# Kernel optimization log

Hardware: AMD Instinct MI355X
Metric: run time of the kernel (lower is better)

The kernel has to match this reference:

```python
import jax, jax.numpy as jnp
import numpy as np

B, NUM, NVAR = 2048, 100, 11
NUM_OBS, NC = 10, 3
T_FIN = 10.0
RHO_OBS = 1.0; RHO_INEQ = 1.0; RHO_LANE = 1.0; RHO_PROJ = 1.0
W_SMOOTH = 20.0; W_VDES = 2.0; W_YDES = 1.0
A_EGO = 3.0; B_EGO = 1.5; MARGIN = 0.2
V_MIN = 0.001; V_MAX = 18.0; A_MAX = 6.0
MAXITER = 5
H = 256

def _basis():
    s = np.linspace(0.0, 1.0, NUM)
    j = np.arange(NVAR)
    P = s[:, None] ** j[None, :]
    Pd = np.zeros((NUM, NVAR)); Pdd = np.zeros((NUM, NVAR))
    Pd[:, 1:] = j[1:][None, :] * s[:, None] ** (j[1:] - 1)[None, :]
    Pdd[:, 2:] = (j[2:] * (j[2:] - 1))[None, :] * s[:, None] ** (j[2:] - 2)[None, :]
    return (jnp.asarray(P, jnp.float32), jnp.asarray(Pd / T_FIN, jnp.float32),
            jnp.asarray(Pdd / (T_FIN ** 2), jnp.float32))

P, PDOT, PDDOT = _basis()
A_EQ_X = jnp.stack([P[0], PDOT[0], PDDOT[0], P[-1]])   # [4, NVAR]
A_EQ_Y = jnp.stack([P[0], PDOT[0], PDDOT[0]])          # [3, NVAR]
PTP = P.T @ P

def _kkt_inv(Q, A):
    m = A.shape[0]
    K = jnp.concatenate([jnp.concatenate([Q, A.T], axis=1),
                         jnp.concatenate([A, jnp.zeros((m, m), jnp.float32)], axis=1)], axis=0)
    return jnp.linalg.inv(K)

# ADMM cost: rho_proj*I + smoothness + rho_obs*A_obs^T A_obs + rho_ineq*(Pdot^T Pdot + Pddot^T Pddot)
Q_COMMON = (RHO_PROJ + W_SMOOTH) * jnp.eye(NVAR, dtype=jnp.float32) \
    + RHO_OBS * NUM_OBS * NC * PTP \
    + RHO_INEQ * (PDOT.T @ PDOT + PDDOT.T @ PDDOT)
KKT_X = _kkt_inv(Q_COMMON, A_EQ_X)
KKT_Y = _kkt_inv(Q_COMMON + 2.0 * RHO_LANE * PTP, A_EQ_Y)   # A_lane = [P; -P]
# x_init QP (smoothness + v_des / y_des tracking)
Q_IX = W_SMOOTH * jnp.eye(NVAR, dtype=jnp.float32) + W_VDES * (PDOT.T @ PDOT)
KKT_IX = _kkt_inv(Q_IX, A_EQ_X)
KKT_IY = _kkt_inv(Q_IX + W_YDES * PTP, A_EQ_Y)


def _forward(init_state_ego, goal_des, closest_obs, psi_obs, dim_x_obs, dim_y_obs,
             y_ub, y_lb, gru_W_ih, gru_W_hh, gru_b, gru_h0,
             mlp_W1, mlp_b1, mlp_W2, mlp_b2):
    b = init_state_ego.shape[0]
    x0, y0, vx0, vy0, ax0, ay0 = (init_state_ego[:, i] for i in range(6))
    b_eq_x = jnp.stack([x0, vx0, ax0, goal_des[:, 0]], axis=1)   # [B,4]
    b_eq_y = jnp.stack([y0, vy0, ay0], axis=1)                    # [B,3]

    # ---- obstacle circle trajectories (static obstacles, vx=vy=0) ----
    xo = closest_obs[:, :NUM_OBS]; yo = closest_obs[:, NUM_OBS:2 * NUM_OBS]   # [B,O]
    r = jnp.stack([jnp.zeros_like(dim_x_obs),
                   (dim_x_obs - dim_y_obs) / 2,
                   -(dim_x_obs - dim_y_obs) / 2], axis=2)                      # [B,O,3]
    x_circ = xo[:, :, None] + r * jnp.cos(psi_obs)[:, :, None]                # [B,O,3]
    y_circ = yo[:, :, None] + r * jnp.sin(psi_obs)[:, :, None]
    shape4 = (b, NUM_OBS, NC, NUM)
    x_obs_f = jnp.broadcast_to(x_circ[..., None], shape4).reshape(b, -1)      # [B,O*C*T]
    y_obs_f = jnp.broadcast_to(y_circ[..., None], shape4).reshape(b, -1)
    rad = dim_y_obs / 2
    a_obs = jnp.broadcast_to((A_EGO + rad + MARGIN)[:, :, None, None], shape4).reshape(b, -1)
    b_obs = jnp.broadcast_to((B_EGO + rad + MARGIN)[:, :, None, None], shape4).reshape(b, -1)

    # ---- GRU context over obstacles -> learned lambda init ----
    feats = jnp.stack([xo, yo, dim_x_obs, dim_y_obs, psi_obs], axis=2)        # [B,O,5]
    def gru_step(h, x):
        gx = x @ gru_W_ih + gru_b
        gh = h @ gru_W_hh
        z = jax.nn.sigmoid(gx[:, :H] + gh[:, :H])
        rg = jax.nn.sigmoid(gx[:, H:2 * H] + gh[:, H:2 * H])
        n = jnp.tanh(gx[:, 2 * H:] + rg * gh[:, 2 * H:])
        return (1.0 - z) * n + z * h, None
    hT, _ = jax.lax.scan(gru_step, jnp.broadcast_to(gru_h0, (b, H)), jnp.swapaxes(feats, 0, 1))
    lam = jax.nn.relu(hT @ mlp_W1 + mlp_b1) @ mlp_W2 + mlp_b2                 # [B,2*NVAR]
    lam_x, lam_y = lam[:, :NVAR], lam[:, NVAR:]

    # ---- x_init: equality-constrained smoothness/tracking QP ----
    v_des = jnp.sqrt(vx0 ** 2 + vy0 ** 2)
    lin_ix = W_VDES * v_des[:, None] * jnp.sum(PDOT, axis=0)[None, :]
    lin_iy = W_YDES * goal_des[:, 1:2] * jnp.sum(P, axis=0)[None, :]
    c_x0 = (jnp.concatenate([lin_ix, b_eq_x], 1) @ KKT_IX.T)[:, :NVAR]
    c_y0 = (jnp.concatenate([lin_iy, b_eq_y], 1) @ KKT_IY.T)[:, :NVAR]

    b_lane = jnp.concatenate([y_ub[:, None] * jnp.ones((1, NUM), jnp.float32),
                              -y_lb[:, None] * jnp.ones((1, NUM), jnp.float32)], axis=1)  # [B,2T]

    def AobsT(v):   # A_obs^T v, v: [B, O*C*T] -> [B, NVAR]
        return v.reshape(b, NUM_OBS * NC, NUM).sum(axis=1) @ P

    def step(carry, _):
        c_x, c_y, lx, ly = carry
        x = c_x @ P.T; xd = c_x @ PDOT.T; xdd = c_x @ PDDOT.T
        y = c_y @ P.T; yd = c_y @ PDOT.T; ydd = c_y @ PDDOT.T
        wc = jnp.tile(x, (1, NUM_OBS * NC)) - x_obs_f
        ws = jnp.tile(y, (1, NUM_OBS * NC)) - y_obs_f
        alpha_o = jnp.arctan2(ws * a_obs, wc * b_obs)
        ca, sa = jnp.cos(alpha_o), jnp.sin(alpha_o)
        c1 = RHO_OBS * (a_obs ** 2 * ca ** 2 + b_obs ** 2 * sa ** 2)
        c2 = RHO_OBS * (a_obs * wc * ca + b_obs * ws * sa)
        d_o = jnp.maximum(1.0, c2 / c1)
        alpha_v = jnp.clip(jnp.arctan2(yd, xd), -0.41, 0.41)
        cv, sv = jnp.cos(alpha_v), jnp.sin(alpha_v)
        d_v = jnp.clip(xd * cv + yd * sv, V_MIN, V_MAX)
        alpha_a = jnp.arctan2(ydd + 1e-4, xdd + 1e-4)
        caa, saa = jnp.cos(alpha_a), jnp.sin(alpha_a)
        d_a = jnp.clip(xdd * caa + ydd * saa, 0.0, A_MAX)
        # targets
        b_ox = x_obs_f + a_obs * d_o * ca; b_oy = y_obs_f + b_obs * d_o * sa
        b_vx = d_v * cv; b_vy = d_v * sv
        b_ax = d_a * caa; b_ay = d_a * saa
        b_lane_aug = jnp.minimum(jnp.concatenate([y, -y], 1), b_lane)  # slack-augmented
        top_x = lx + RHO_PROJ * c_x0 + RHO_OBS * AobsT(b_ox) + RHO_INEQ * (b_vx @ PDOT + b_ax @ PDDOT)
        top_y = ly + RHO_PROJ * c_y0 + RHO_OBS * AobsT(b_oy) + RHO_INEQ * (b_vy @ PDOT + b_ay @ PDDOT) \
            + RHO_LANE * ((b_lane_aug[:, :NUM] - b_lane_aug[:, NUM:]) @ P)
        c_xn = (jnp.concatenate([top_x, b_eq_x], 1) @ KKT_X.T)[:, :NVAR]
        c_yn = (jnp.concatenate([top_y, b_eq_y], 1) @ KKT_Y.T)[:, :NVAR]
        # residuals / Lagrange multiplier updates
        xn = c_xn @ P.T; yn = c_yn @ P.T
        res_ox = jnp.tile(xn, (1, NUM_OBS * NC)) - b_ox
        res_oy = jnp.tile(yn, (1, NUM_OBS * NC)) - b_oy
        lxn = lx - RHO_OBS * AobsT(res_ox) \
            - RHO_INEQ * ((c_xn @ PDOT.T - b_vx) @ PDOT + (c_xn @ PDDOT.T - b_ax) @ PDDOT)
        res_lane = jnp.concatenate([yn, -yn], 1) - b_lane_aug
        lyn = ly - RHO_OBS * AobsT(res_oy) \
            - RHO_INEQ * ((c_yn @ PDOT.T - b_vy) @ PDOT + (c_yn @ PDDOT.T - b_ay) @ PDDOT) \
            - RHO_LANE * ((res_lane[:, :NUM] - res_lane[:, NUM:]) @ P)
        return (c_xn, c_yn, lxn, lyn), None

    (c_x, c_y, lam_x, lam_y), _ = jax.lax.scan(step, (c_x0, c_y0, lam_x, lam_y),
                                               None, length=MAXITER)
    return jnp.concatenate([c_x, c_y], axis=1)   # [B, 2*NVAR]


def setup_inputs() -> dict:
    key = jax.random.key(0)
    ks = jax.random.split(key, 12)
    d = {
        'init_state_ego': jax.random.normal(ks[0], (B, 6), jnp.float32),
        'goal_des': jax.random.normal(ks[1], (B, 2), jnp.float32),
        'closest_obs': jax.random.normal(ks[2], (B, 2 * NUM_OBS), jnp.float32),
        'psi_obs': jax.random.normal(ks[3], (B, NUM_OBS), jnp.float32),
        'dim_x_obs': jax.random.uniform(ks[4], (B, NUM_OBS), jnp.float32),
        'dim_y_obs': jax.random.uniform(ks[5], (B, NUM_OBS), jnp.float32),
        'y_ub': jnp.ones((B,), jnp.float32),
        'y_lb': jnp.zeros((B,), jnp.float32),
        'gru_W_ih': jax.random.normal(ks[6], (5, 3 * H), jnp.float32) / np.sqrt(5.0),
        'gru_W_hh': jax.random.normal(ks[7], (H, 3 * H), jnp.float32) / np.sqrt(float(H)),
        'gru_b': jnp.zeros((3 * H,), jnp.float32),
        'gru_h0': jax.random.normal(ks[8], (H,), jnp.float32) * 0.1,
        'mlp_W1': jax.random.normal(ks[9], (H, 512), jnp.float32) / np.sqrt(float(H)),
        'mlp_b1': jnp.zeros((512,), jnp.float32),
        'mlp_W2': jax.random.normal(ks[10], (512, 2 * NVAR), jnp.float32) / np.sqrt(512.0),
        'mlp_b2': jnp.zeros((2 * NVAR,), jnp.float32),
    }
    return d


def reference(init_state_ego, goal_des, closest_obs, psi_obs, dim_x_obs, dim_y_obs,
              y_ub, y_lb, gru_W_ih, gru_W_hh, gru_b, gru_h0,
              mlp_W1, mlp_b1, mlp_W2, mlp_b2):
    return _forward(init_state_ego, goal_des, closest_obs, psi_obs, dim_x_obs, dim_y_obs,
                    y_ub, y_lb, gru_W_ih, gru_W_hh, gru_b, gru_h0,
                    mlp_W1, mlp_b1, mlp_W2, mlp_b2)
```

## Files before the change

### kernel.cpp

```cpp
#include <hip/hip_runtime.h>
#include <math.h>

typedef short bf16x8 __attribute__((ext_vector_type(8)));
typedef float f32x4 __attribute__((ext_vector_type(4)));

__device__ __forceinline__ unsigned short f2bf(float x) {
  union { float f; unsigned u; } v; v.f = x;
  unsigned r = v.u + 0x7FFFu + ((v.u >> 16) & 1u);
  return (unsigned short)(r >> 16);
}
__device__ __forceinline__ float bf2f(unsigned short h) {
  union { unsigned u; float f; } v; v.u = ((unsigned)h) << 16; return v.f;
}

#define WS_WAUG  0u
#define WS_W1T   442368u
#define WS_HAUGA 704512u
#define WS_HAUGB 1884160u
#define WS_HF32  3063808u
#define WS_ACTS  3063808u
#define WS_LAM   5160960u
#define WS_KKT   5341184u
#define WS_GX    5344000u
#define WS_GY    5344704u
#define WS_MX    5345408u
#define WS_MY    5346112u
#define WS_SUMS  5346816u

__global__ __launch_bounds__(256) void prep(
    const float* __restrict__ Whh, const float* __restrict__ Wih,
    const float* __restrict__ gb, const float* __restrict__ W1,
    const float* __restrict__ h0,
    const float* __restrict__ obs, const float* __restrict__ dimx,
    const float* __restrict__ dimy, const float* __restrict__ psi,
    unsigned short* __restrict__ Waug, unsigned short* __restrict__ W1T,
    unsigned short* __restrict__ HaugA, unsigned short* __restrict__ HaugB,
    float* __restrict__ kkt_out, float* __restrict__ Gx_out,
    float* __restrict__ Gy_out, float* __restrict__ Mx_out,
    float* __restrict__ My_out, float* __restrict__ sums_out)
{
  __shared__ double S[21];
  __shared__ double aug[15][32];
  __shared__ double fbuf[15];
  __shared__ double Md[11][11];
  if (blockIdx.x < 4) {
    const int mat = blockIdx.x;
    const int n = (mat == 0 || mat == 2) ? 15 : 14;
    const int twoN = 2 * n;
    if (threadIdx.x == 0) {
      for (int m = 0; m < 21; ++m) S[m] = 0.0;
      for (int s = 0; s < 100; ++s) {
        double t = s * (1.0 / 99.0);
        double p = 1.0;
        for (int m = 0; m < 21; ++m) { S[m] += p; p *= t; }
      }
    }
    __syncthreads();
    for (int idx = threadIdx.x; idx < n * twoN; idx += 256) {
      int r = idx / twoN, c = idx % twoN;
      double v;
      if (c >= n) v = (c - n == r) ? 1.0 : 0.0;
      else if (r < 11 && c < 11) {
        double ptp = S[r + c];
        double pdp = (r >= 1 && c >= 1) ? ((double)(r * c) / 100.0) * S[r + c - 2] : 0.0;
        double pddp = (r >= 2 && c >= 2) ? ((double)(r*(r-1)) * (double)(c*(c-1)) / 10000.0) * S[r + c - 4] : 0.0;
        double dg = (r == c) ? 1.0 : 0.0;
        if (mat == 0)      v = 21.0*dg + 30.0*ptp + pdp + pddp;
        else if (mat == 1) v = 21.0*dg + 32.0*ptp + pdp + pddp;
        else if (mat == 2) v = 20.0*dg + 2.0*pdp;
        else               v = 20.0*dg + 2.0*pdp + ptp;
      } else if (r >= 11 && c >= 11) v = 0.0;
      else {
        int ar = (r >= 11) ? (r - 11) : (c - 11);
        int ac = (r >= 11) ? c : r;
        v = (ar == 0) ? ((ac == 0) ? 1.0 : 0.0)
          : (ar == 1) ? ((ac == 1) ? 0.1 : 0.0)
          : (ar == 2) ? ((ac == 2) ? 0.02 : 0.0)
          : 1.0;
      }
      aug[r][c] = v;
    }
    __syncthreads();
    for (int p = 0; p < n; ++p) {
      double pv = aug[p][p];
      __syncthreads();
      double inv = 1.0 / pv;
      for (int c = threadIdx.x; c < twoN; c += 256) aug[p][c] *= inv;
      __syncthreads();
      if (threadIdx.x < n) fbuf[threadIdx.x] = aug[threadIdx.x][p];
      __syncthreads();
      for (int idx = threadIdx.x; idx < n * twoN; idx += 256) {
        int r = idx / twoN, c = idx % twoN;
        if (r != p) aug[r][c] -= fbuf[r] * aug[p][c];
      }
      __syncthreads();
    }
    for (int idx = threadIdx.x; idx < 11 * n; idx += 256) {
      int r = idx / n, c = idx % n;
      kkt_out[mat * 176 + r * 16 + c] = (float)aug[r][n + c];
    }
    if (mat < 2) {
      if (threadIdx.x < 121) {
        int j = threadIdx.x / 11, i = threadIdx.x % 11;
        double m = 30.0 * S[j + i];
        if (j >= 1 && i >= 1) m += ((double)(j * i) / 100.0) * S[j + i - 2];
        if (j >= 2 && i >= 2) m += ((double)(j*(j-1)) * (double)(i*(i-1)) / 10000.0) * S[j + i - 4];
        if (mat == 1) m += 2.0 * S[j + i];
        Md[j][i] = m;
      }
      __syncthreads();
      if (threadIdx.x < 121) {
        int j = threadIdx.x / 11, i = threadIdx.x % 11;
        double g = (j == i) ? 1.0 : 0.0;
        for (int k = 0; k < 11; ++k) g -= Md[j][k] * aug[k][n + i];
        if (mat == 0) { Gx_out[j * 16 + i] = (float)g; Mx_out[j * 16 + i] = (float)Md[j][i]; }
        else          { Gy_out[j * 16 + i] = (float)g; My_out[j * 16 + i] = (float)Md[j][i]; }
      }
    }
    if (mat == 0 && threadIdx.x < 11) {
      int j = threadIdx.x;
      sums_out[j] = (float)S[j];
      sums_out[11 + j] = (j >= 1) ? (float)((double)j / 10.0 * S[j - 1]) : 0.f;
    }
    return;
  }
  int idx = (blockIdx.x - 4) * 256 + threadIdx.x;
  if (idx < 221184) {
    int col = idx / 288, k = idx - col * 288;
    float v;
    if (k < 256)       v = Whh[k * 768 + col];
    else if (k < 261)  v = Wih[(k - 256) * 768 + col];
    else if (k == 261) v = gb[col];
    else               v = 0.f;
    Waug[idx] = f2bf(v);
  } else if (idx < 352256) {
    int j = idx - 221184;
    int col = j >> 8, k = j & 255;
    W1T[j] = f2bf(W1[k * 512 + col]);
  } else if (idx < 942080) {
    int j = idx - 352256;
    int row = j / 288, k = j - row * 288;
    float v;
    if (k < 256)       v = h0[k];
    else if (k == 256) v = obs[row * 20 + 0];
    else if (k == 257) v = obs[row * 20 + 10];
    else if (k == 258) v = dimx[row * 10 + 0];
    else if (k == 259) v = dimy[row * 10 + 0];
    else if (k == 260) v = psi[row * 10 + 0];
    else if (k == 261) v = 1.0f;
    else               v = 0.f;
    HaugA[row * 288 + k] = f2bf(v);
  } else if (idx < 995328) {
    int j = idx - 942080;
    int row = j / 26, k = 262 + (j - row * 26);
    HaugB[row * 288 + k] = 0;
  }
}

#define MFMA __builtin_amdgcn_mfma_f32_16x16x32_bf16
__global__ __launch_bounds__(256) void gru_step(
    const unsigned short* __restrict__ Waug,
    const unsigned short* __restrict__ HaugC, unsigned short* __restrict__ HaugN,
    float* __restrict__ Hf32, const float* __restrict__ h0,
    const float* __restrict__ obs, const float* __restrict__ dimx,
    const float* __restrict__ dimy, const float* __restrict__ psi,
    int s)
{
  const int tid = threadIdx.x;
  const int m0 = blockIdx.x * 32;
  const int c0 = blockIdx.y * 32;
  const int lane = tid & 63, w = tid >> 6;
  const int l15 = lane & 15, g4 = lane >> 4;
  const int mi = w >> 1, cg = w & 1;

  const unsigned short* Arow = HaugC + (size_t)(m0 + mi * 16 + l15) * 288 + g4 * 8;
  const unsigned short* Bcol = Waug + (size_t)(c0 + cg * 16 + l15) * 288 + g4 * 8;

  f32x4 accz = {0.f,0.f,0.f,0.f}, accr = {0.f,0.f,0.f,0.f};
  f32x4 anh = {0.f,0.f,0.f,0.f}, anx = {0.f,0.f,0.f,0.f};

  #pragma unroll
  for (int kc = 0; kc < 9; ++kc) {
    bf16x8 a  = *(const bf16x8*)(Arow + kc * 32);
    bf16x8 bz = *(const bf16x8*)(Bcol + kc * 32);
    bf16x8 br = *(const bf16x8*)(Bcol + 256 * 288 + kc * 32);
    bf16x8 bn = *(const bf16x8*)(Bcol + 512 * 288 + kc * 32);
    accz = MFMA(a, bz, accz, 0, 0, 0);
    accr = MFMA(a, br, accr, 0, 0, 0);
    if (kc < 8) anh = MFMA(a, bn, anh, 0, 0, 0);
    else        anx = MFMA(a, bn, anx, 0, 0, 0);
  }

  const int colh = c0 + cg * 16 + l15;
  float h0c = (s == 0) ? h0[colh] : 0.f;
  #pragma unroll
  for (int rg = 0; rg < 4; ++rg) {
    int row = m0 + mi * 16 + g4 * 4 + rg;
    float hold = (s == 0) ? h0c : Hf32[(size_t)row * 256 + colh];
    float z = 1.f / (1.f + __expf(-accz[rg]));
    float rr = 1.f / (1.f + __expf(-accr[rg]));
    float nn = tanhf(anx[rg] + rr * anh[rg]);
    float hnew = (1.f - z) * nn + z * hold;
    Hf32[(size_t)row * 256 + colh] = hnew;
    HaugN[(size_t)row * 288 + colh] = f2bf(hnew);
  }
  if (blockIdx.y == 0 && s < 9 && tid < 192) {
    int row = m0 + tid / 6, e = tid - (tid / 6) * 6;
    int s1 = s + 1;
    float v = (e == 0) ? obs[row * 20 + s1] : (e == 1) ? obs[row * 20 + 10 + s1]
            : (e == 2) ? dimx[row * 10 + s1] : (e == 3) ? dimy[row * 10 + s1]
            : (e == 4) ? psi[row * 10 + s1] : 1.0f;
    HaugN[(size_t)row * 288 + 256 + e] = f2bf(v);
  }
}

__global__ __launch_bounds__(256) void mlp1(
    const unsigned short* __restrict__ Haug, const unsigned short* __restrict__ W1T,
    const float* __restrict__ b1, unsigned short* __restrict__ acts)
{
  __shared__ __align__(16) unsigned short As[8192];
  const int tid = threadIdx.x;
  const int m0 = blockIdx.x * 32, c0 = blockIdx.y * 128;
  const int lane = tid & 63, w = tid >> 6, l15 = lane & 15, g4 = lane >> 4;

  #pragma unroll
  for (int r = 0; r < 4; ++r) {
    int j = tid + 256 * r;
    int tile = j >> 6, q = j & 63, ci = q >> 2, ks = q & 3;
    int mi = tile >> 3, kc = tile & 7;
    const unsigned short* src = Haug + (size_t)(m0 + mi * 16 + ci) * 288 + kc * 32 + ks * 8;
    *(int4*)&As[tile * 512 + q * 8] = *(const int4*)src;
  }
  __syncthreads();

  const int foff = (l15 * 4 + g4) * 8;
  f32x4 acc[2][2];
  #pragma unroll
  for (int a = 0; a < 2; ++a)
    #pragma unroll
    for (int b = 0; b < 2; ++b) acc[a][b] = (f32x4){0.f,0.f,0.f,0.f};

  #pragma unroll
  for (int kc = 0; kc < 8; ++kc) {
    bf16x8 a0 = *(const bf16x8*)&As[(0 * 8 + kc) * 512 + foff];
    bf16x8 a1 = *(const bf16x8*)&As[(1 * 8 + kc) * 512 + foff];
    int kk = kc * 32 + g4 * 8;
    #pragma unroll
    for (int nt = 0; nt < 2; ++nt) {
      int col = c0 + w * 32 + nt * 16 + l15;
      bf16x8 b = *(const bf16x8*)&W1T[(size_t)col * 256 + kk];
      acc[0][nt] = MFMA(a0, b, acc[0][nt], 0, 0, 0);
      acc[1][nt] = MFMA(a1, b, acc[1][nt], 0, 0, 0);
    }
  }
  #pragma unroll
  for (int mi = 0; mi < 2; ++mi)
    #pragma unroll
    for (int nt = 0; nt < 2; ++nt) {
      int col = c0 + w * 32 + nt * 16 + l15;
      float bb = b1[col];
      #pragma unroll
      for (int rg = 0; rg < 4; ++rg) {
        int row = m0 + mi * 16 + g4 * 4 + rg;
        float v = fmaxf(acc[mi][nt][rg] + bb, 0.f);
        acts[(size_t)row * 512 + col] = f2bf(v);
      }
    }
}

__global__ __launch_bounds__(256) void mlp2(
    const unsigned short* __restrict__ acts, const float* __restrict__ W2,
    const float* __restrict__ b2, float* __restrict__ lam)
{
  __shared__ unsigned short Ablk[8 * 520];
  __shared__ float W2s[512 * 22];
  const int tid = threadIdx.x;
  const int m0 = blockIdx.x * 8;
  for (int i = tid; i < 4096; i += 256) {
    int r = i >> 9, k = i & 511;
    Ablk[r * 520 + k] = acts[(size_t)(m0 + r) * 512 + k];
  }
  for (int i = tid; i < 11264; i += 256) W2s[i] = W2[i];
  __syncthreads();
  if (tid < 176) {
    int row = tid / 22, col = tid - (tid / 22) * 22;
    float s = b2[col];
    const unsigned short* ap = &Ablk[row * 520];
    for (int k = 0; k < 512; ++k) s += bf2f(ap[k]) * W2s[k * 22 + col];
    lam[(size_t)(m0 + row) * 22 + col] = s;
  }
}

__global__ __launch_bounds__(128) void solver(
    const float* __restrict__ ise, const float* __restrict__ goal,
    const float* __restrict__ obs, const float* __restrict__ psi,
    const float* __restrict__ dimx, const float* __restrict__ dimy,
    const float* __restrict__ yub, const float* __restrict__ ylb,
    const float* __restrict__ lam, const float* __restrict__ kkt,
    const float* __restrict__ Gxm, const float* __restrict__ Gym,
    const float* __restrict__ Mxm, const float* __restrict__ Mym,
    const float* __restrict__ sums, float* __restrict__ out)
{
  __shared__ __align__(16) float Pt[3][11][108];
  __shared__ __align__(16) float red[7][108];
  __shared__ float redout[7][11];
  __shared__ float cx[11], cy[11], lx[11], ly[11], cx0[11], cy0[11];
  __shared__ float kxB[11], kyB[11], hx[11], hy[11];
  __shared__ float rhsx[15], rhsy[14];
  __shared__ float xc[30], yc[30], sa_[10], sb_[10], sab[10], sab2[10];

  const int b = blockIdx.x;
  const int tid = threadIdx.x;

  if (tid < 100) {
    float t = tid * (1.0f / 99.0f);
    float tjm2 = 0.f, tjm1 = 0.f, tj = 1.f;
    #pragma unroll
    for (int j = 0; j < 11; ++j) {
      Pt[0][j][tid] = tj;
      Pt[1][j][tid] = 0.1f * (float)j * tjm1;
      Pt[2][j][tid] = 0.01f * (float)(j * (j - 1)) * tjm2;
      tjm2 = tjm1; tjm1 = tj; tj *= t;
    }
  }
  if (tid < 10) {
    int o = tid;
    float xo = obs[b * 20 + o], yo = obs[b * 20 + 10 + o];
    float dx = dimx[b * 10 + o], dy = dimy[b * 10 + o], ps = psi[b * 10 + o];
    float sp, cp;
    __sincosf(ps, &sp, &cp);
    float r1 = 0.5f * (dx - dy);
    xc[o * 3] = xo; xc[o * 3 + 1] = xo + r1 * cp; xc[o * 3 + 2] = xo - r1 * cp;
    yc[o * 3] = yo; yc[o * 3 + 1] = yo + r1 * sp; yc[o * 3 + 2] = yo - r1 * sp;
    float rad = 0.5f * dy;
    float av = 3.2f + rad, bv = 1.7f + rad;
    sa_[o] = av; sb_[o] = bv; sab[o] = av * bv; sab2[o] = av * bv * av * bv;
  }
  if (tid < 11) { lx[tid] = lam[b * 22 + tid]; ly[tid] = lam[b * 22 + 11 + tid]; }
  const float vx0 = ise[b * 6 + 2], vy0 = ise[b * 6 + 3];
  if (tid == 0) {
    float x0 = ise[b * 6 + 0], y0 = ise[b * 6 + 1];
    float ax0 = ise[b * 6 + 4], ay0 = ise[b * 6 + 5];
    rhsx[11] = x0; rhsx[12] = vx0; rhsx[13] = ax0; rhsx[14] = goal[b * 2 + 0];
    rhsy[11] = y0; rhsy[12] = vy0; rhsy[13] = ay0;
  }
  {
    float vdes = sqrtf(vx0 * vx0 + vy0 * vy0);
    float gy = goal[b * 2 + 1];
    if (tid < 11) { rhsx[tid] = 2.f * vdes * sums[11 + tid]; rhsy[tid] = gy * sums[tid]; }
  }
  const float yU = yub[b], yL = ylb[b];
  __syncthreads();
  if (tid < 11) {
    const float* K = kkt + 2 * 176 + tid * 16;
    float s = 0.f;
    #pragma unroll
    for (int j = 0; j < 15; ++j) s += K[j] * rhsx[j];
    cx0[tid] = s; cx[tid] = s;
    const float* Kx = kkt + tid * 16;
    float kb = 0.f;
    #pragma unroll
    for (int c = 0; c < 4; ++c) kb += Kx[11 + c] * rhsx[11 + c];
    kxB[tid] = kb;
  } else if (tid >= 16 && tid < 27) {
    int i = tid - 16;
    const float* K = kkt + 3 * 176 + i * 16;
    float s = 0.f;
    #pragma unroll
    for (int j = 0; j < 14; ++j) s += K[j] * rhsy[j];
    cy0[i] = s; cy[i] = s;
    const float* Ky = kkt + 176 + i * 16;
    float kb = 0.f;
    #pragma unroll
    for (int c = 0; c < 3; ++c) kb += Ky[11 + c] * rhsy[11 + c];
    kyB[i] = kb;
  }
  __syncthreads();
  if (tid < 11) {
    float s = cx0[tid];
    #pragma unroll
    for (int i = 0; i < 11; ++i) s += Mxm[tid * 16 + i] * kxB[i];
    hx[tid] = s;
  } else if (tid >= 16 && tid < 27) {
    int j = tid - 16;
    float s = cy0[j];
    #pragma unroll
    for (int i = 0; i < 11; ++i) s += Mym[j * 16 + i] * kyB[i];
    hy[j] = s;
  }
  __syncthreads();

  for (int it = 0; it < 5; ++it) {
    if (tid < 100) {
      float t = tid * (1.0f / 99.0f);
      float x = 0, y = 0, xd = 0, yd = 0, xdd = 0, ydd = 0;
      {
        float tjm2 = 0, tjm1 = 0, tj = 1;
        #pragma unroll
        for (int j = 0; j < 11; ++j) {
          float cj = cx[j], dj = cy[j];
          x += cj * tj; y += dj * tj;
          float pd = 0.1f * (float)j * tjm1;
          xd += cj * pd; yd += dj * pd;
          float pdd = 0.01f * (float)(j * (j - 1)) * tjm2;
          xdd += cj * pdd; ydd += dj * pdd;
          tjm2 = tjm1; tjm1 = tj; tj *= t;
        }
      }
      float Sbx = 0.f, Sby = 0.f;
      for (int oi = 0; oi < 10; ++oi) {
        float A = sa_[oi], B = sb_[oi], AB = sab[oi], AB2 = sab2[oi];
        #pragma unroll
        for (int cc = 0; cc < 3; ++cc) {
          int o = oi * 3 + cc;
          float xcc = xc[o], ycc = yc[o];
          float wc = x - xcc, wsv = y - ycc;
          float p = wsv * A, q = wc * B;
          float h2 = p * p + q * q;
          float rin = rsqrtf(h2 + 1e-20f);
          float sc = AB * rin;
          bool outside = h2 >= AB2;
          Sbx += outside ? x : fmaf(wc, sc, xcc);
          Sby += outside ? y : fmaf(wsv, sc, ycc);
        }
      }
      bool clipv = (xd <= 0.f) || (fabsf(yd) > xd * 0.43463135f);
      float cv, sv;
      if (clipv) { cv = 0.91712081f; sv = copysignf(0.39860934f, yd); }
      else { float ri = rsqrtf(fmaxf(xd * xd + yd * yd, 1e-24f)); cv = xd * ri; sv = yd * ri; }
      float dv = fminf(fmaxf(xd * cv + yd * sv, 0.001f), 18.f);
      float qa = xdd + 1e-4f, pa = ydd + 1e-4f;
      float ria = rsqrtf(pa * pa + qa * qa + 1e-30f);
      float caa = qa * ria, saa = pa * ria;
      float da = fminf(fmaxf(xdd * caa + ydd * saa, 0.f), 6.f);
      red[0][tid] = Sbx; red[1][tid] = Sby;
      red[2][tid] = dv * cv; red[3][tid] = dv * sv;
      red[4][tid] = da * caa; red[5][tid] = da * saa;
      red[6][tid] = fminf(y, yU) - fminf(-y, -yL);
    }
    __syncthreads();
    if (tid < 77) {
      int a = tid / 11, j = tid - a * 11;
      int wt = (a < 2) ? 0 : (a < 4) ? 1 : (a < 6) ? 2 : 0;
      const float4* rp = (const float4*)(&red[a][0]);
      const float4* wp = (const float4*)(&Pt[wt][j][0]);
      float s = 0.f;
      #pragma unroll
      for (int k = 0; k < 25; ++k) {
        float4 rv = rp[k], wv = wp[k];
        s += rv.x * wv.x + rv.y * wv.y + rv.z * wv.z + rv.w * wv.w;
      }
      redout[a][j] = s;
    }
    __syncthreads();
    if (tid < 11) rhsx[tid] = lx[tid] + cx0[tid] + redout[0][tid] + redout[2][tid] + redout[4][tid];
    else if (tid >= 16 && tid < 27) {
      int j = tid - 16;
      rhsy[j] = ly[j] + cy0[j] + redout[1][j] + redout[3][j] + redout[5][j] + redout[6][j];
    }
    __syncthreads();
    if (tid < 11) {
      const float* K = kkt + tid * 16;
      const float* G = Gxm + tid * 16;
      float sc = kxB[tid], sl = -hx[tid];
      #pragma unroll
      for (int i = 0; i < 11; ++i) {
        float r = rhsx[i];
        sc += K[i] * r;
        sl += G[i] * r;
      }
      cx[tid] = sc; lx[tid] = sl;
    } else if (tid >= 16 && tid < 27) {
      int j = tid - 16;
      const float* K = kkt + 176 + j * 16;
      const float* G = Gym + j * 16;
      float sc = kyB[j], sl = -hy[j];
      #pragma unroll
      for (int i = 0; i < 11; ++i) {
        float r = rhsy[i];
        sc += K[i] * r;
        sl += G[i] * r;
      }
      cy[j] = sc; ly[j] = sl;
    }
    __syncthreads();
  }
  if (tid < 11) out[b * 22 + tid] = cx[tid];
  else if (tid >= 16 && tid < 27) out[b * 22 + 11 + (tid - 16)] = cy[tid - 16];
}

extern "C" void kernel_launch(void* const* d_in, const int* in_sizes, int n_in,
                              void* d_out, int out_size, void* d_ws, size_t ws_size,
                              hipStream_t stream) {
  const float* ise  = (const float*)d_in[0];
  const float* goal = (const float*)d_in[1];
  const float* obs  = (const float*)d_in[2];
  const float* psi  = (const float*)d_in[3];
  const float* dimx = (const float*)d_in[4];
  const float* dimy = (const float*)d_in[5];
  const float* yub  = (const float*)d_in[6];
  const float* ylb  = (const float*)d_in[7];
  const float* Wih  = (const float*)d_in[8];
  const float* Whh  = (const float*)d_in[9];
  const float* gb   = (const float*)d_in[10];
  const float* h0   = (const float*)d_in[11];
  const float* W1   = (const float*)d_in[12];
  const float* b1   = (const float*)d_in[13];
  const float* W2   = (const float*)d_in[14];
  const float* b2   = (const float*)d_in[15];

  char* ws = (char*)d_ws;
  unsigned short* Waug  = (unsigned short*)(ws + WS_WAUG);
  unsigned short* W1T   = (unsigned short*)(ws + WS_W1T);
  unsigned short* HaugA = (unsigned short*)(ws + WS_HAUGA);
  unsigned short* HaugB = (unsigned short*)(ws + WS_HAUGB);
  float* Hf32 = (float*)(ws + WS_HF32);
  unsigned short* acts = (unsigned short*)(ws + WS_ACTS);
  float* lamb = (float*)(ws + WS_LAM);
  float* kkt  = (float*)(ws + WS_KKT);
  float* Gxm  = (float*)(ws + WS_GX);
  float* Gym  = (float*)(ws + WS_GY);
  float* Mxm  = (float*)(ws + WS_MX);
  float* Mym  = (float*)(ws + WS_MY);
  float* sums = (float*)(ws + WS_SUMS);

  prep<<<3892, 256, 0, stream>>>(Whh, Wih, gb, W1, h0, obs, dimx, dimy, psi,
                                 Waug, W1T, HaugA, HaugB, kkt, Gxm, Gym, Mxm, Mym, sums);
  for (int s = 0; s < 10; ++s) {
    const unsigned short* hc = (s & 1) ? HaugB : HaugA;
    unsigned short* hn = (s & 1) ? HaugA : HaugB;
    gru_step<<<dim3(64, 8), 256, 0, stream>>>(Waug, hc, hn, Hf32, h0,
                                              obs, dimx, dimy, psi, s);
  }
  mlp1<<<dim3(64, 4), 256, 0, stream>>>(HaugA, W1T, b1, acts);
  mlp2<<<256, 256, 0, stream>>>(acts, W2, b2, lamb);
  solver<<<2048, 128, 0, stream>>>(ise, goal, obs, psi, dimx, dimy, yub, ylb,
                                   lamb, kkt, Gxm, Gym, Mxm, Mym, sums, (float*)d_out);
  (void)in_sizes; (void)n_in; (void)out_size; (void)ws_size;
}
```

Baseline: 245.3 us.

## Fuse GRU steps and MLP into one persistent kernel with grid barriers

Replaces the ten per-step GRU launches plus the two MLP launches with a single 256-block persistent kernel. Steps are separated by an atomic-counter grid barrier, which removes eleven kernel launches and their gaps. The solver now runs 256 threads, and the extra threads compute half of the obstacle projection sums, which shortens the serial per-thread loop. The power-sum setup in prep is also parallelised, and one syncthreads in the solver is dropped by computing the RHS inline. The grid barrier assumes all 256 blocks are co-resident, and it adds spin-wait and fence overhead at each step.

```diff
diff --git a/kernel.cpp b/kernel.cpp
--- a/kernel.cpp
+++ b/kernel.cpp
@@ -26,6 +26,19 @@
 #define WS_MX    5345408u
 #define WS_MY    5346112u
 #define WS_SUMS  5346816u
+#define WS_BAR   5346944u
+
+__device__ __forceinline__ void gridbar(unsigned int* ctr, unsigned int target) {
+  __threadfence();
+  __syncthreads();
+  if (threadIdx.x == 0) {
+    __hip_atomic_fetch_add(ctr, 1u, __ATOMIC_ACQ_REL, __HIP_MEMORY_SCOPE_AGENT);
+    while (__hip_atomic_load(ctr, __ATOMIC_ACQUIRE, __HIP_MEMORY_SCOPE_AGENT) < target)
+      __builtin_amdgcn_s_sleep(1);
+  }
+  __syncthreads();
+  __threadfence();
+}
 
 __global__ __launch_bounds__(256) void prep(
     const float* __restrict__ Whh, const float* __restrict__ Wih,
@@ -37,23 +50,29 @@
     unsigned short* __restrict__ HaugA, unsigned short* __restrict__ HaugB,
     float* __restrict__ kkt_out, float* __restrict__ Gx_out,
     float* __restrict__ Gy_out, float* __restrict__ Mx_out,
-    float* __restrict__ My_out, float* __restrict__ sums_out)
+    float* __restrict__ My_out, float* __restrict__ sums_out,
+    unsigned int* __restrict__ bar)
 {
   __shared__ double S[21];
+  __shared__ double Spow[21][104];
   __shared__ double aug[15][32];
   __shared__ double fbuf[15];
   __shared__ double Md[11][11];
+  if (blockIdx.x == 0 && threadIdx.x == 0) bar[0] = 0u;
   if (blockIdx.x < 4) {
     const int mat = blockIdx.x;
     const int n = (mat == 0 || mat == 2) ? 15 : 14;
     const int twoN = 2 * n;
-    if (threadIdx.x == 0) {
-      for (int m = 0; m < 21; ++m) S[m] = 0.0;
-      for (int s = 0; s < 100; ++s) {
-        double t = s * (1.0 / 99.0);
-        double p = 1.0;
-        for (int m = 0; m < 21; ++m) { S[m] += p; p *= t; }
-      }
+    if (threadIdx.x < 100) {
+      double t = threadIdx.x * (1.0 / 99.0);
+      double p = 1.0;
+      for (int m = 0; m < 21; ++m) { Spow[m][threadIdx.x] = p; p *= t; }
+    }
+    __syncthreads();
+    if (threadIdx.x < 21) {
+      double s = 0.0;
+      for (int k = 0; k < 100; ++k) s += Spow[threadIdx.x][k];
+      S[threadIdx.x] = s;
     }
     __syncthreads();
     for (int idx = threadIdx.x; idx < n * twoN; idx += 256) {
@@ -158,140 +177,149 @@
 }
 
 #define MFMA __builtin_amdgcn_mfma_f32_16x16x32_bf16
-__global__ __launch_bounds__(256) void gru_step(
+__global__ __launch_bounds__(256) void nn_all(
     const unsigned short* __restrict__ Waug,
-    const unsigned short* __restrict__ HaugC, unsigned short* __restrict__ HaugN,
+    unsigned short* __restrict__ HaugA, unsigned short* __restrict__ HaugB,
     float* __restrict__ Hf32, const float* __restrict__ h0,
     const float* __restrict__ obs, const float* __restrict__ dimx,
     const float* __restrict__ dimy, const float* __restrict__ psi,
-    int s)
+    const unsigned short* __restrict__ W1T, const float* __restrict__ b1,
+    const float* __restrict__ W2, const float* __restrict__ b2,
+    unsigned short* __restrict__ acts, float* __restrict__ lam,
+    unsigned int* __restrict__ bar)
 {
+  __shared__ __align__(16) unsigned char smem[53376];
   const int tid = threadIdx.x;
-  const int m0 = blockIdx.x * 32;
-  const int c0 = blockIdx.y * 32;
+  const int bid = blockIdx.x;
   const int lane = tid & 63, w = tid >> 6;
   const int l15 = lane & 15, g4 = lane >> 4;
-  const int mi = w >> 1, cg = w & 1;
-
-  const unsigned short* Arow = HaugC + (size_t)(m0 + mi * 16 + l15) * 288 + g4 * 8;
-  const unsigned short* Bcol = Waug + (size_t)(c0 + cg * 16 + l15) * 288 + g4 * 8;
-
-  f32x4 accz = {0.f,0.f,0.f,0.f}, accr = {0.f,0.f,0.f,0.f};
-  f32x4 anh = {0.f,0.f,0.f,0.f}, anx = {0.f,0.f,0.f,0.f};
-
-  #pragma unroll
-  for (int kc = 0; kc < 9; ++kc) {
-    bf16x8 a  = *(const bf16x8*)(Arow + kc * 32);
-    bf16x8 bz = *(const bf16x8*)(Bcol + kc * 32);
-    bf16x8 br = *(const bf16x8*)(Bcol + 256 * 288 + kc * 32);
-    bf16x8 bn = *(const bf16x8*)(Bcol + 512 * 288 + kc * 32);
-    accz = MFMA(a, bz, accz, 0, 0, 0);
-    accr = MFMA(a, br, accr, 0, 0, 0);
-    if (kc < 8) anh = MFMA(a, bn, anh, 0, 0, 0);
-    else        anx = MFMA(a, bn, anx, 0, 0, 0);
-  }
-
-  const int colh = c0 + cg * 16 + l15;
-  float h0c = (s == 0) ? h0[colh] : 0.f;
-  #pragma unroll
-  for (int rg = 0; rg < 4; ++rg) {
-    int row = m0 + mi * 16 + g4 * 4 + rg;
-    float hold = (s == 0) ? h0c : Hf32[(size_t)row * 256 + colh];
-    float z = 1.f / (1.f + __expf(-accz[rg]));
-    float rr = 1.f / (1.f + __expf(-accr[rg]));
-    float nn = tanhf(anx[rg] + rr * anh[rg]);
-    float hnew = (1.f - z) * nn + z * hold;
-    Hf32[(size_t)row * 256 + colh] = hnew;
-    HaugN[(size_t)row * 288 + colh] = f2bf(hnew);
-  }
-  if (blockIdx.y == 0 && s < 9 && tid < 192) {
-    int row = m0 + tid / 6, e = tid - (tid / 6) * 6;
-    int s1 = s + 1;
-    float v = (e == 0) ? obs[row * 20 + s1] : (e == 1) ? obs[row * 20 + 10 + s1]
-            : (e == 2) ? dimx[row * 10 + s1] : (e == 3) ? dimy[row * 10 + s1]
-            : (e == 4) ? psi[row * 10 + s1] : 1.0f;
-    HaugN[(size_t)row * 288 + 256 + e] = f2bf(v);
-  }
-}
-
-__global__ __launch_bounds__(256) void mlp1(
-    const unsigned short* __restrict__ Haug, const unsigned short* __restrict__ W1T,
-    const float* __restrict__ b1, unsigned short* __restrict__ acts)
-{
-  __shared__ __align__(16) unsigned short As[8192];
-  const int tid = threadIdx.x;
-  const int m0 = blockIdx.x * 32, c0 = blockIdx.y * 128;
-  const int lane = tid & 63, w = tid >> 6, l15 = lane & 15, g4 = lane >> 4;
-
-  #pragma unroll
-  for (int r = 0; r < 4; ++r) {
-    int j = tid + 256 * r;
-    int tile = j >> 6, q = j & 63, ci = q >> 2, ks = q & 3;
-    int mi = tile >> 3, kc = tile & 7;
-    const unsigned short* src = Haug + (size_t)(m0 + mi * 16 + ci) * 288 + kc * 32 + ks * 8;
-    *(int4*)&As[tile * 512 + q * 8] = *(const int4*)src;
-  }
-  __syncthreads();
-
-  const int foff = (l15 * 4 + g4) * 8;
-  f32x4 acc[2][2];
-  #pragma unroll
-  for (int a = 0; a < 2; ++a)
-    #pragma unroll
-    for (int b = 0; b < 2; ++b) acc[a][b] = (f32x4){0.f,0.f,0.f,0.f};
-
-  #pragma unroll
-  for (int kc = 0; kc < 8; ++kc) {
-    bf16x8 a0 = *(const bf16x8*)&As[(0 * 8 + kc) * 512 + foff];
-    bf16x8 a1 = *(const bf16x8*)&As[(1 * 8 + kc) * 512 + foff];
-    int kk = kc * 32 + g4 * 8;
-    #pragma unroll
-    for (int nt = 0; nt < 2; ++nt) {
-      int col = c0 + w * 32 + nt * 16 + l15;
-      bf16x8 b = *(const bf16x8*)&W1T[(size_t)col * 256 + kk];
-      acc[0][nt] = MFMA(a0, b, acc[0][nt], 0, 0, 0);
-      acc[1][nt] = MFMA(a1, b, acc[1][nt], 0, 0, 0);
-    }
-  }
-  #pragma unroll
-  for (int mi = 0; mi < 2; ++mi)
-    #pragma unroll
-    for (int nt = 0; nt < 2; ++nt) {
-      int col = c0 + w * 32 + nt * 16 + l15;
-      float bb = b1[col];
-      #pragma unroll
-      for (int rg = 0; rg < 4; ++rg) {
-        int row = m0 + mi * 16 + g4 * 4 + rg;
-        float v = fmaxf(acc[mi][nt][rg] + bb, 0.f);
-        acts[(size_t)row * 512 + col] = f2bf(v);
-      }
-    }
-}
-
-__global__ __launch_bounds__(256) void mlp2(
-    const unsigned short* __restrict__ acts, const float* __restrict__ W2,
-    const float* __restrict__ b2, float* __restrict__ lam)
-{
-  __shared__ unsigned short Ablk[8 * 520];
-  __shared__ float W2s[512 * 22];
-  const int tid = threadIdx.x;
-  const int m0 = blockIdx.x * 8;
-  for (int i = tid; i < 4096; i += 256) {
-    int r = i >> 9, k = i & 511;
-    Ablk[r * 520 + k] = acts[(size_t)(m0 + r) * 512 + k];
-  }
-  for (int i = tid; i < 11264; i += 256) W2s[i] = W2[i];
-  __syncthreads();
-  if (tid < 176) {
-    int row = tid / 22, col = tid - (tid / 22) * 22;
-    float s = b2[col];
-    const unsigned short* ap = &Ablk[row * 520];
-    for (int k = 0; k < 512; ++k) s += bf2f(ap[k]) * W2s[k * 22 + col];
-    lam[(size_t)(m0 + row) * 22 + col] = s;
-  }
-}
-
-__global__ __launch_bounds__(128) void solver(
+
+  {
+    const int m0 = (bid >> 2) * 32;
+    const int c0 = (bid & 3) * 64;
+    const int cw = c0 + w * 16 + l15;
+    const float h0c = h0[cw];
+    for (int s = 0; s < 10; ++s) {
+      const unsigned short* HaugC = (s & 1) ? HaugB : HaugA;
+      unsigned short* HaugN = (s & 1) ? HaugA : HaugB;
+      const unsigned short* Arow0 = HaugC + (size_t)(m0 + l15) * 288 + g4 * 8;
+      const unsigned short* Arow1 = HaugC + (size_t)(m0 + 16 + l15) * 288 + g4 * 8;
+      const unsigned short* Bc = Waug + (size_t)cw * 288 + g4 * 8;
+      f32x4 az0 = {0.f,0.f,0.f,0.f}, az1 = {0.f,0.f,0.f,0.f};
+      f32x4 ar0 = {0.f,0.f,0.f,0.f}, ar1 = {0.f,0.f,0.f,0.f};
+      f32x4 nh0 = {0.f,0.f,0.f,0.f}, nh1 = {0.f,0.f,0.f,0.f};
+      f32x4 nx0 = {0.f,0.f,0.f,0.f}, nx1 = {0.f,0.f,0.f,0.f};
+      #pragma unroll
+      for (int kc = 0; kc < 9; ++kc) {
+        bf16x8 a0 = *(const bf16x8*)(Arow0 + kc * 32);
+        bf16x8 a1 = *(const bf16x8*)(Arow1 + kc * 32);
+        bf16x8 bz = *(const bf16x8*)(Bc + kc * 32);
+        bf16x8 br = *(const bf16x8*)(Bc + 256 * 288 + kc * 32);
+        bf16x8 bn = *(const bf16x8*)(Bc + 512 * 288 + kc * 32);
+        az0 = MFMA(a0, bz, az0, 0, 0, 0);
+        az1 = MFMA(a1, bz, az1, 0, 0, 0);
+        ar0 = MFMA(a0, br, ar0, 0, 0, 0);
+        ar1 = MFMA(a1, br, ar1, 0, 0, 0);
+        if (kc < 8) { nh0 = MFMA(a0, bn, nh0, 0, 0, 0); nh1 = MFMA(a1, bn, nh1, 0, 0, 0); }
+        else        { nx0 = MFMA(a0, bn, nx0, 0, 0, 0); nx1 = MFMA(a1, bn, nx1, 0, 0, 0); }
+      }
+      #pragma unroll
+      for (int mi = 0; mi < 2; ++mi) {
+        f32x4 az = mi ? az1 : az0, arr = mi ? ar1 : ar0;
+        f32x4 nh = mi ? nh1 : nh0, nx = mi ? nx1 : nx0;
+        #pragma unroll
+        for (int rg = 0; rg < 4; ++rg) {
+          int row = m0 + mi * 16 + g4 * 4 + rg;
+          float hold = (s == 0) ? h0c : Hf32[(size_t)row * 256 + cw];
+          float z = 1.f / (1.f + __expf(-az[rg]));
+          float rr = 1.f / (1.f + __expf(-arr[rg]));
+          float nn = tanhf(nx[rg] + rr * nh[rg]);
+          float hnew = (1.f - z) * nn + z * hold;
+          Hf32[(size_t)row * 256 + cw] = hnew;
+          HaugN[(size_t)row * 288 + cw] = f2bf(hnew);
+        }
+      }
+      if ((bid & 3) == 0 && s < 9 && tid < 192) {
+        int row = m0 + tid / 6, e = tid - (tid / 6) * 6;
+        int s1 = s + 1;
+        float v = (e == 0) ? obs[row * 20 + s1] : (e == 1) ? obs[row * 20 + 10 + s1]
+                : (e == 2) ? dimx[row * 10 + s1] : (e == 3) ? dimy[row * 10 + s1]
+                : (e == 4) ? psi[row * 10 + s1] : 1.0f;
+        HaugN[(size_t)row * 288 + 256 + e] = f2bf(v);
+      }
+      gridbar(bar, 256u * (unsigned)(s + 1));
+    }
+  }
+
+  {
+    unsigned short* As = (unsigned short*)smem;
+    const int m0 = (bid >> 2) * 32, c0 = (bid & 3) * 128;
+    #pragma unroll
+    for (int r = 0; r < 4; ++r) {
+      int j = tid + 256 * r;
+      int tile = j >> 6, q = j & 63, ci = q >> 2, ks = q & 3;
+      int mi = tile >> 3, kc = tile & 7;
+      const unsigned short* src = HaugA + (size_t)(m0 + mi * 16 + ci) * 288 + kc * 32 + ks * 8;
+      *(int4*)&As[tile * 512 + q * 8] = *(const int4*)src;
+    }
+    __syncthreads();
+    const int foff = (l15 * 4 + g4) * 8;
+    f32x4 acc[2][2];
+    #pragma unroll
+    for (int a = 0; a < 2; ++a)
+      #pragma unroll
+      for (int b = 0; b < 2; ++b) acc[a][b] = (f32x4){0.f,0.f,0.f,0.f};
+    #pragma unroll
+    for (int kc = 0; kc < 8; ++kc) {
+      bf16x8 a0 = *(const bf16x8*)&As[(0 * 8 + kc) * 512 + foff];
+      bf16x8 a1 = *(const bf16x8*)&As[(1 * 8 + kc) * 512 + foff];
+      int kk = kc * 32 + g4 * 8;
+      #pragma unroll
+      for (int nt = 0; nt < 2; ++nt) {
+        int col = c0 + w * 32 + nt * 16 + l15;
+        bf16x8 b = *(const bf16x8*)&W1T[(size_t)col * 256 + kk];
+        acc[0][nt] = MFMA(a0, b, acc[0][nt], 0, 0, 0);
+        acc[1][nt] = MFMA(a1, b, acc[1][nt], 0, 0, 0);
+      }
+    }
+    #pragma unroll
+    for (int mi = 0; mi < 2; ++mi)
+      #pragma unroll
+      for (int nt = 0; nt < 2; ++nt) {
+        int col = c0 + w * 32 + nt * 16 + l15;
+        float bb = b1[col];
+        #pragma unroll
+        for (int rg = 0; rg < 4; ++rg) {
+          int row = m0 + mi * 16 + g4 * 4 + rg;
+          float v = fmaxf(acc[mi][nt][rg] + bb, 0.f);
+          acts[(size_t)row * 512 + col] = f2bf(v);
+        }
+      }
+    gridbar(bar, 256u * 11u);
+  }
+
+  {
+    unsigned short* Ablk = (unsigned short*)smem;
+    float* W2s = (float*)(smem + 8320);
+    const int m0 = bid * 8;
+    __syncthreads();
+    for (int i = tid; i < 4096; i += 256) {
+      int r = i >> 9, k = i & 511;
+      Ablk[r * 520 + k] = acts[(size_t)(m0 + r) * 512 + k];
+    }
+    for (int i = tid; i < 11264; i += 256) W2s[i] = W2[i];
+    __syncthreads();
+    if (tid < 176) {
+      int row = tid / 22, col = tid - (tid / 22) * 22;
+      float s = b2[col];
+      const unsigned short* ap = &Ablk[row * 520];
+      for (int k = 0; k < 512; ++k) s += bf2f(ap[k]) * W2s[k * 22 + col];
+      lam[(size_t)(m0 + row) * 22 + col] = s;
+    }
+  }
+}
+
+__global__ __launch_bounds__(256) void solver(
     const float* __restrict__ ise, const float* __restrict__ goal,
     const float* __restrict__ obs, const float* __restrict__ psi,
     const float* __restrict__ dimx, const float* __restrict__ dimy,
@@ -303,6 +331,7 @@
 {
   __shared__ __align__(16) float Pt[3][11][108];
   __shared__ __align__(16) float red[7][108];
+  __shared__ __align__(16) float red2[2][108];
   __shared__ float redout[7][11];
   __shared__ float cx[11], cy[11], lx[11], ly[11], cx0[11], cy0[11];
   __shared__ float kxB[11], kyB[11], hx[11], hy[11];
@@ -408,7 +437,7 @@
         }
       }
       float Sbx = 0.f, Sby = 0.f;
-      for (int oi = 0; oi < 10; ++oi) {
+      for (int oi = 0; oi < 5; ++oi) {
         float A = sa_[oi], B = sb_[oi], AB = sab[oi], AB2 = sab2[oi];
         #pragma unroll
         for (int cc = 0; cc < 3; ++cc) {
@@ -437,6 +466,33 @@
       red[2][tid] = dv * cv; red[3][tid] = dv * sv;
       red[4][tid] = da * caa; red[5][tid] = da * saa;
       red[6][tid] = fminf(y, yU) - fminf(-y, -yL);
+    } else if (tid >= 128 && tid < 228) {
+      int t2 = tid - 128;
+      float t = t2 * (1.0f / 99.0f);
+      float x = 0, y = 0;
+      {
+        float tj = 1;
+        #pragma unroll
+        for (int j = 0; j < 11; ++j) { x += cx[j] * tj; y += cy[j] * tj; tj *= t; }
+      }
+      float Sbx = 0.f, Sby = 0.f;
+      for (int oi = 5; oi < 10; ++oi) {
+        float A = sa_[oi], B = sb_[oi], AB = sab[oi], AB2 = sab2[oi];
+        #pragma unroll
+        for (int cc = 0; cc < 3; ++cc) {
+          int o = oi * 3 + cc;
+          float xcc = xc[o], ycc = yc[o];
+          float wc = x - xcc, wsv = y - ycc;
+          float p = wsv * A, q = wc * B;
+          float h2 = p * p + q * q;
+          float rin = rsqrtf(h2 + 1e-20f);
+          float sc = AB * rin;
+          bool outside = h2 >= AB2;
+          Sbx += outside ? x : fmaf(wc, sc, xcc);
+          Sby += outside ? y : fmaf(wsv, sc, ycc);
+        }
+      }
+      red2[0][t2] = Sbx; red2[1][t2] = Sby;
     }
     __syncthreads();
     if (tid < 77) {
@@ -445,18 +501,22 @@
       const float4* rp = (const float4*)(&red[a][0]);
       const float4* wp = (const float4*)(&Pt[wt][j][0]);
       float s = 0.f;
-      #pragma unroll
-      for (int k = 0; k < 25; ++k) {
-        float4 rv = rp[k], wv = wp[k];
-        s += rv.x * wv.x + rv.y * wv.y + rv.z * wv.z + rv.w * wv.w;
+      if (a < 2) {
+        const float4* r2p = (const float4*)(&red2[a][0]);
+        #pragma unroll
+        for (int k = 0; k < 25; ++k) {
+          float4 rv = rp[k], r2 = r2p[k], wv = wp[k];
+          s += (rv.x + r2.x) * wv.x + (rv.y + r2.y) * wv.y
+             + (rv.z + r2.z) * wv.z + (rv.w + r2.w) * wv.w;
+        }
+      } else {
+        #pragma unroll
+        for (int k = 0; k < 25; ++k) {
+          float4 rv = rp[k], wv = wp[k];
+          s += rv.x * wv.x + rv.y * wv.y + rv.z * wv.z + rv.w * wv.w;
+        }
       }
       redout[a][j] = s;
-    }
-    __syncthreads();
-    if (tid < 11) rhsx[tid] = lx[tid] + cx0[tid] + redout[0][tid] + redout[2][tid] + redout[4][tid];
-    else if (tid >= 16 && tid < 27) {
-      int j = tid - 16;
-      rhsy[j] = ly[j] + cy0[j] + redout[1][j] + redout[3][j] + redout[5][j] + redout[6][j];
     }
     __syncthreads();
     if (tid < 11) {
@@ -465,7 +525,7 @@
       float sc = kxB[tid], sl = -hx[tid];
       #pragma unroll
       for (int i = 0; i < 11; ++i) {
-        float r = rhsx[i];
+        float r = lx[i] + cx0[i] + redout[0][i] + redout[2][i] + redout[4][i];
         sc += K[i] * r;
         sl += G[i] * r;
       }
@@ -477,7 +537,7 @@
       float sc = kyB[j], sl = -hy[j];
       #pragma unroll
       for (int i = 0; i < 11; ++i) {
-        float r = rhsy[i];
+        float r = ly[i] + cy0[i] + redout[1][i] + redout[3][i] + redout[5][i] + redout[6][i];
         sc += K[i] * r;
         sl += G[i] * r;
       }
@@ -523,18 +583,15 @@
   float* Mxm  = (float*)(ws + WS_MX);
   float* Mym  = (float*)(ws + WS_MY);
   float* sums = (float*)(ws + WS_SUMS);
+  unsigned int* bar = (unsigned int*)(ws + WS_BAR);
 
   prep<<<3892, 256, 0, stream>>>(Whh, Wih, gb, W1, h0, obs, dimx, dimy, psi,
-                                 Waug, W1T, HaugA, HaugB, kkt, Gxm, Gym, Mxm, Mym, sums);
-  for (int s = 0; s < 10; ++s) {
-    const unsigned short* hc = (s & 1) ? HaugB : HaugA;
-    unsigned short* hn = (s & 1) ? HaugA : HaugB;
-    gru_step<<<dim3(64, 8), 256, 0, stream>>>(Waug, hc, hn, Hf32, h0,
-                                              obs, dimx, dimy, psi, s);
-  }
-  mlp1<<<dim3(64, 4), 256, 0, stream>>>(HaugA, W1T, b1, acts);
-  mlp2<<<256, 256, 0, stream>>>(acts, W2, b2, lamb);
-  solver<<<2048, 128, 0, stream>>>(ise, goal, obs, psi, dimx, dimy, yub, ylb,
+                                 Waug, W1T, HaugA, HaugB, kkt, Gxm, Gym, Mxm, Mym,
+                                 sums, bar);
+  nn_all<<<256, 256, 0, stream>>>(Waug, HaugA, HaugB, Hf32, h0,
+                                  obs, dimx, dimy, psi, W1T, b1, W2, b2,
+                                  acts, lamb, bar);
+  solver<<<2048, 256, 0, stream>>>(ise, goal, obs, psi, dimx, dimy, yub, ylb,
                                    lamb, kkt, Gxm, Gym, Mxm, Mym, sums, (float*)d_out);
   (void)in_sizes; (void)n_in; (void)out_size; (void)ws_size;
 }
```

Result: slower. 962.0 us (+292.2%).
